# Kernel tuning notes

Measured on AMD Instinct MI355X. Metric: run time of the kernel, lower is better.

The kernel has to match this reference:

```python
import jax, jax.numpy as jnp
import numpy as np

N = 40000      # nodes
E = 640000     # edges
F_IN = 128     # feature_dim
HID = 256      # hidden_dim
OUT = 128      # out_dim
B = 64         # num graphs
HEADS = 4
EPS = 1e-5


def setup_inputs() -> dict:
    key = jax.random.key(0)
    ks = jax.random.split(key, 32)
    s = 0.02
    inp = {
        "x_bb_masked": jax.random.normal(ks[0], (N, F_IN), jnp.float32),
        "x_att_masked": jax.random.normal(ks[1], (N, F_IN), jnp.float32),
        # SAGEConv1: in->hid  (lin_l acts on mean-aggregated neighbors, lin_r on root)
        "W1l": jax.random.normal(ks[2], (HID, F_IN), jnp.float32) * s,
        "b1l": jnp.zeros((HID,), jnp.float32),
        "W1r": jax.random.normal(ks[3], (HID, F_IN), jnp.float32) * s,
        # SAGEConv2: hid->hid
        "W2l": jax.random.normal(ks[4], (HID, HID), jnp.float32) * s,
        "b2l": jnp.zeros((HID,), jnp.float32),
        "W2r": jax.random.normal(ks[5], (HID, HID), jnp.float32) * s,
        # SAGEConv3: hid->out
        "W3l": jax.random.normal(ks[6], (OUT, HID), jnp.float32) * s,
        "b3l": jnp.zeros((OUT,), jnp.float32),
        "W3r": jax.random.normal(ks[7], (OUT, HID), jnp.float32) * s,
        # cross-attention projections
        "Wq": jax.random.normal(ks[8], (HID, F_IN), jnp.float32) * s,
        "bq": jnp.zeros((HID,), jnp.float32),
        "Wk": jax.random.normal(ks[9], (HID, OUT), jnp.float32) * s,
        "bk": jnp.zeros((HID,), jnp.float32),
        "Wv": jax.random.normal(ks[10], (HID, OUT), jnp.float32) * s,
        "bv": jnp.zeros((HID,), jnp.float32),
        # nn.MultiheadAttention packed in-proj and out-proj
        "in_proj_w": jax.random.normal(ks[11], (3 * HID, HID), jnp.float32) * s,
        "in_proj_b": jnp.zeros((3 * HID,), jnp.float32),
        "out_w": jax.random.normal(ks[12], (HID, HID), jnp.float32) * s,
        "out_b": jnp.zeros((HID,), jnp.float32),
        "ln_g": jnp.ones((HID,), jnp.float32),
        "ln_b": jnp.zeros((HID,), jnp.float32),
        "edge_index": jax.random.randint(ks[13], (2, E), 0, N, jnp.int64),
        "batch": jnp.sort(jax.random.randint(ks[14], (N,), 0, B, jnp.int64)),
    }
    return inp


def _sage(x, src, dst, Wl, bl, Wr):
    # mean aggregation of source features at target nodes, then lin_l(agg)+lin_r(x)
    agg = jax.ops.segment_sum(x[src], dst, num_segments=N)          # [N, d]
    cnt = jax.ops.segment_sum(jnp.ones((src.shape[0],), x.dtype), dst, num_segments=N)
    mean = agg / jnp.maximum(cnt, 1.0)[:, None]
    return mean @ Wl.T + bl + x @ Wr.T


def _forward(x_bb_masked, x_att_masked,
             W1l, b1l, W1r, W2l, b2l, W2r, W3l, b3l, W3r,
             Wq, bq, Wk, bk, Wv, bv, in_proj_w, in_proj_b, out_w, out_b,
             ln_g, ln_b, edge_index, batch):
    src, dst = edge_index[0], edge_index[1]
    h = jax.nn.relu(_sage(x_bb_masked, src, dst, W1l, b1l, W1r))
    h = jax.nn.relu(_sage(h, src, dst, W2l, b2l, W2r))
    h = _sage(h, src, dst, W3l, b3l, W3r)                           # [N, OUT]
    # global mean pool per graph
    gsum = jax.ops.segment_sum(h, batch, num_segments=B)            # [B, OUT]
    gcnt = jax.ops.segment_sum(jnp.ones((N,), h.dtype), batch, num_segments=B)
    graph_vec = gsum / jnp.maximum(gcnt, 1.0)[:, None]

    # cross attention: query per node, key/value from its graph vector (seq_len = 1)
    query = x_att_masked @ Wq.T + bq                                # [N, HID]
    gv = graph_vec[batch]                                           # [N, OUT]
    keyt = gv @ Wk.T + bk
    val = gv @ Wv.T + bv
    q = query @ in_proj_w[:HID].T + in_proj_b[:HID]
    k = keyt @ in_proj_w[HID:2 * HID].T + in_proj_b[HID:2 * HID]
    v = val @ in_proj_w[2 * HID:].T + in_proj_b[2 * HID:]
    dh = HID // HEADS
    qh = q.reshape(N, HEADS, dh)
    kh = k.reshape(N, HEADS, dh)
    vh = v.reshape(N, HEADS, dh)
    scores = jnp.sum(qh * kh, axis=-1, keepdims=True) / jnp.sqrt(jnp.asarray(dh, q.dtype))
    w = jax.nn.softmax(scores, axis=-1)                             # length-1 kv -> ones
    attn = (w * vh).reshape(N, HID)
    attn = attn @ out_w.T + out_b
    # LayerNorm
    mu = jnp.mean(attn, axis=-1, keepdims=True)
    var = jnp.mean((attn - mu) ** 2, axis=-1, keepdims=True)
    node_embeddings = (attn - mu) / jnp.sqrt(var + EPS) * ln_g + ln_b
    return graph_vec, node_embeddings


def reference(x_bb_masked, x_att_masked,
              W1l, b1l, W1r, W2l, b2l, W2r, W3l, b3l, W3r,
              Wq, bq, Wk, bk, Wv, bv, in_proj_w, in_proj_b, out_w, out_b,
              ln_g, ln_b, edge_index, batch):
    return _forward(x_bb_masked, x_att_masked,
                    W1l, b1l, W1r, W2l, b2l, W2r, W3l, b3l, W3r,
                    Wq, bq, Wk, bk, Wv, bv, in_proj_w, in_proj_b, out_w, out_b,
                    ln_g, ln_b, edge_index, batch)
```

## Files before the change

kernel.cpp:

```cpp
#include <hip/hip_runtime.h>

#define N_NODES 40000
#define N_EDGES 640000
#define NGRAPH 64

typedef unsigned short u16;
typedef unsigned char u8;
typedef unsigned int u32;
typedef __attribute__((ext_vector_type(2))) float floatx2;
typedef __attribute__((ext_vector_type(4))) float floatx4;
typedef __attribute__((ext_vector_type(8))) short short8;
typedef __attribute__((ext_vector_type(8))) __bf16 bf16x8;

__device__ __forceinline__ float bf2f(u16 u) {
  u32 x = ((u32)u) << 16;
  return __builtin_bit_cast(float, x);
}
__device__ __forceinline__ u16 f2bf(float f) {
  u32 u = __builtin_bit_cast(u32, f);
  u += 0x7fffu + ((u >> 16) & 1u);
  return (u16)(u >> 16);
}
__device__ __forceinline__ uint2 f4tob(float4 v) {
  u32 lo = (u32)f2bf(v.x) | ((u32)f2bf(v.y) << 16);
  u32 hi = (u32)f2bf(v.z) | ((u32)f2bf(v.w) << 16);
  return make_uint2(lo, hi);
}
__device__ __forceinline__ u32 fp8pk_lo(float a, float b, u32 old) {
  return (u32)__builtin_amdgcn_cvt_pk_fp8_f32(a, b, (int)old, false);
}
__device__ __forceinline__ u32 fp8pk_hi(float a, float b, u32 old) {
  return (u32)__builtin_amdgcn_cvt_pk_fp8_f32(a, b, (int)old, true);
}
__device__ __forceinline__ floatx2 fp8up_lo(u32 v) {
  return __builtin_amdgcn_cvt_pk_f32_fp8((int)v, false);
}
__device__ __forceinline__ floatx2 fp8up_hi(u32 v) {
  return __builtin_amdgcn_cvt_pk_f32_fp8((int)v, true);
}
__device__ __forceinline__ void gld16(const void* g, void* l) {
  __builtin_amdgcn_global_load_lds(
      (const __attribute__((address_space(1))) u32*)g,
      (__attribute__((address_space(3))) u32*)l, 16, 0, 0);
}

__global__ __launch_bounds__(256) void k_setup(const float* __restrict__ x_bb, u16* __restrict__ xb,
                                               u8* __restrict__ xq,
                                               const float* __restrict__ W1l, u16* __restrict__ w1l,
                                               const float* __restrict__ W1r, u16* __restrict__ w1r,
                                               const float* __restrict__ W2l, u16* __restrict__ w2l,
                                               const float* __restrict__ W2r, u16* __restrict__ w2r,
                                               const float* __restrict__ W3l, u16* __restrict__ w3s,
                                               const float* __restrict__ W3r, u16* __restrict__ w3r,
                                               int* __restrict__ zbase,
                                               const int* __restrict__ batch, int* __restrict__ gstart) {
  const int tid = blockIdx.x * 256 + threadIdx.x;
  const int nth = gridDim.x * 256;
  for (int i = tid; i < 2 * N_NODES + 8192; i += nth) zbase[i] = 0;
  for (int i = tid; i < N_NODES * 32; i += nth) {
    float4 v = ((const float4*)x_bb)[i];
    ((uint2*)xb)[i] = f4tob(v);
    if (xq) {
      u32 q = fp8pk_lo(v.x, v.y, 0);
      q = fp8pk_hi(v.z, v.w, q);
      ((u32*)xq)[i] = q;
    }
  }
  for (int i = tid; i < 65536; i += nth) {
    const float* s; u16* d; int off;
    if (i < 8192)       { s = W1l; d = w1l; off = i; }
    else if (i < 16384) { s = W1r; d = w1r; off = i - 8192; }
    else if (i < 32768) { s = W2l; d = w2l; off = i - 16384; }
    else if (i < 49152) { s = W2r; d = w2r; off = i - 32768; }
    else if (i < 57344) { s = W3l; d = w3s; off = i - 49152; }
    else                { s = W3r; d = w3r; off = i - 57344; }
    ((uint2*)d)[off] = f4tob(((const float4*)s)[off]);
  }
  if (tid <= NGRAPH) {
    int lo = 0, hi = N_NODES;
    while (lo < hi) { int mid = (lo + hi) >> 1; if (batch[mid] < tid) lo = mid + 1; else hi = mid; }
    gstart[tid] = lo;
  }
}

__global__ void k_hist(const int* __restrict__ ei, int* __restrict__ cnt) {
  int e = blockIdx.x * 256 + threadIdx.x;
  int d = ei[N_EDGES + e];
  atomicAdd(&cnt[d], 1);
}
__global__ void k_blocksum(const int* __restrict__ cnt, int* __restrict__ bsum, int n) {
  __shared__ int s[256];
  int t = threadIdx.x, i = blockIdx.x * 256 + t;
  s[t] = (i < n) ? cnt[i] : 0;
  __syncthreads();
  for (int off = 128; off > 0; off >>= 1) {
    if (t < off) s[t] += s[t + off];
    __syncthreads();
  }
  if (t == 0) bsum[blockIdx.x] = s[0];
}
__global__ void k_scan_small(int* bsum, int n) {
  __shared__ int s[256];
  int t = threadIdx.x;
  int orig = (t < n) ? bsum[t] : 0;
  s[t] = orig;
  __syncthreads();
  for (int off = 1; off < 256; off <<= 1) {
    int v = (t >= off) ? s[t - off] : 0;
    __syncthreads();
    s[t] += v;
    __syncthreads();
  }
  if (t < n) bsum[t] = s[t] - orig;
}
__global__ void k_rowptr(const int* __restrict__ cnt, const int* __restrict__ bsum,
                         int* __restrict__ rowptr, float* __restrict__ invc, int n, int total) {
  __shared__ int s[256];
  int t = threadIdx.x, i = blockIdx.x * 256 + t;
  int c = (i < n) ? cnt[i] : 0;
  s[t] = c;
  __syncthreads();
  for (int off = 1; off < 256; off <<= 1) {
    int v = (t >= off) ? s[t - off] : 0;
    __syncthreads();
    s[t] += v;
    __syncthreads();
  }
  if (i < n) {
    rowptr[i] = bsum[blockIdx.x] + s[t] - c;
    invc[i] = 1.0f / (float)(c > 1 ? c : 1);
  }
  if (i == 0) rowptr[n] = total;
}
__global__ void k_scatter(const int* __restrict__ ei, const int* __restrict__ rowptr,
                          int* __restrict__ cursor, int* __restrict__ perm) {
  int e = blockIdx.x * 256 + threadIdx.x;
  int d = ei[N_EDGES + e];
  int srcn = ei[e];
  int pos = rowptr[d] + atomicAdd(&cursor[d], 1);
  perm[pos] = srcn;
}

template <int D, int MODE, int QT>
__global__ __launch_bounds__(256) void k_agg(const void* __restrict__ xv, u16* __restrict__ outp,
                                             const int* __restrict__ rowptr,
                                             const int* __restrict__ perm,
                                             const float* __restrict__ invc,
                                             const u16* __restrict__ Radd, int nn) {
  int wv = threadIdx.x >> 6, lane = threadIdx.x & 63;
  int node = blockIdx.x * 4 + wv;
  if (node >= nn) return;
  int s = rowptr[node], e = rowptr[node + 1];
  int slot = lane >> 4, lsub = lane & 15;
  constexpr int FR = D / 16;
  float acc[FR];
#pragma unroll
  for (int i = 0; i < FR; ++i) acc[i] = 0.f;

  int p = s + slot;
  if constexpr (QT == 1) {
    const u8* xl = (const u8*)xv + lsub * FR;
    constexpr int NW = FR / 4;
    for (; p + 4 < e; p += 8) {
      int s0 = perm[p], s1 = perm[p + 4];
      const u8* r0 = xl + (size_t)s0 * D;
      const u8* r1 = xl + (size_t)s1 * D;
      u32 wa[NW], wb[NW];
      if constexpr (D == 128) {
        uint2 a = *(const uint2*)r0; wa[0] = a.x; wa[1] = a.y;
        uint2 b = *(const uint2*)r1; wb[0] = b.x; wb[1] = b.y;
      } else {
        uint4 a = *(const uint4*)r0; wa[0] = a.x; wa[1] = a.y; wa[2] = a.z; wa[3] = a.w;
        uint4 b = *(const uint4*)r1; wb[0] = b.x; wb[1] = b.y; wb[2] = b.z; wb[3] = b.w;
      }
#pragma unroll
      for (int j = 0; j < NW; ++j) {
        floatx2 l0 = fp8up_lo(wa[j]), h0 = fp8up_hi(wa[j]);
        floatx2 l1 = fp8up_lo(wb[j]), h1 = fp8up_hi(wb[j]);
        acc[4 * j]     += l0[0] + l1[0];
        acc[4 * j + 1] += l0[1] + l1[1];
        acc[4 * j + 2] += h0[0] + h1[0];
        acc[4 * j + 3] += h0[1] + h1[1];
      }
    }
    if (p < e) {
      int s0 = perm[p];
      const u8* r0 = xl + (size_t)s0 * D;
      u32 wa[NW];
      if constexpr (D == 128) {
        uint2 a = *(const uint2*)r0; wa[0] = a.x; wa[1] = a.y;
      } else {
        uint4 a = *(const uint4*)r0; wa[0] = a.x; wa[1] = a.y; wa[2] = a.z; wa[3] = a.w;
      }
#pragma unroll
      for (int j = 0; j < NW; ++j) {
        floatx2 l0 = fp8up_lo(wa[j]), h0 = fp8up_hi(wa[j]);
        acc[4 * j]     += l0[0];
        acc[4 * j + 1] += l0[1];
        acc[4 * j + 2] += h0[0];
        acc[4 * j + 3] += h0[1];
      }
    }
  } else {
    const u16* xl = (const u16*)xv + lsub * FR;
    for (; p + 4 < e; p += 8) {
      int src0 = perm[p];
      int src1 = perm[p + 4];
      const u16* rp0 = xl + (size_t)src0 * D;
      const u16* rp1 = xl + (size_t)src1 * D;
      if (D == 128) {
        uint4 va = *(const uint4*)rp0;
        uint4 vb = *(const uint4*)rp1;
        u32 wa[4] = {va.x, va.y, va.z, va.w}, wb[4] = {vb.x, vb.y, vb.z, vb.w};
#pragma unroll
        for (int j = 0; j < 4; ++j) {
          acc[2 * j] += __builtin_bit_cast(float, wa[j] << 16) + __builtin_bit_cast(float, wb[j] << 16);
          acc[2 * j + 1] += __builtin_bit_cast(float, wa[j] & 0xffff0000u) + __builtin_bit_cast(float, wb[j] & 0xffff0000u);
        }
      } else {
        uint4 a0 = *(const uint4*)rp0;
        uint4 a1 = *(const uint4*)(rp0 + 8);
        uint4 b0 = *(const uint4*)rp1;
        uint4 b1 = *(const uint4*)(rp1 + 8);
        u32 wa[8] = {a0.x, a0.y, a0.z, a0.w, a1.x, a1.y, a1.z, a1.w};
        u32 wb[8] = {b0.x, b0.y, b0.z, b0.w, b1.x, b1.y, b1.z, b1.w};
#pragma unroll
        for (int j = 0; j < 8; ++j) {
          acc[2 * j] += __builtin_bit_cast(float, wa[j] << 16) + __builtin_bit_cast(float, wb[j] << 16);
          acc[2 * j + 1] += __builtin_bit_cast(float, wa[j] & 0xffff0000u) + __builtin_bit_cast(float, wb[j] & 0xffff0000u);
        }
      }
    }
    if (p < e) {
      int src = perm[p];
      const u16* rp = xl + (size_t)src * D;
      if (D == 128) {
        uint4 va = *(const uint4*)rp;
        u32 wa[4] = {va.x, va.y, va.z, va.w};
#pragma unroll
        for (int j = 0; j < 4; ++j) {
          acc[2 * j] += __builtin_bit_cast(float, wa[j] << 16);
          acc[2 * j + 1] += __builtin_bit_cast(float, wa[j] & 0xffff0000u);
        }
      } else {
        uint4 a0 = *(const uint4*)rp;
        uint4 a1 = *(const uint4*)(rp + 8);
        u32 wa[8] = {a0.x, a0.y, a0.z, a0.w, a1.x, a1.y, a1.z, a1.w};
#pragma unroll
        for (int j = 0; j < 8; ++j) {
          acc[2 * j] += __builtin_bit_cast(float, wa[j] << 16);
          acc[2 * j + 1] += __builtin_bit_cast(float, wa[j] & 0xffff0000u);
        }
      }
    }
  }

#pragma unroll
  for (int i = 0; i < FR; ++i) {
    acc[i] += __shfl_xor(acc[i], 16, 64);
    acc[i] += __shfl_xor(acc[i], 32, 64);
  }

  if (slot == 0) {
    float iv = invc[node];
    float v[FR];
#pragma unroll
    for (int i = 0; i < FR; ++i) v[i] = acc[i] * iv;
    if (MODE == 1) {
      const uint4* rr = (const uint4*)(Radd + (size_t)node * D + lsub * FR);
      uint4 va = rr[0];
      u32 wa[4] = {va.x, va.y, va.z, va.w};
#pragma unroll
      for (int j = 0; j < 4; ++j) {
        v[2 * j] += __builtin_bit_cast(float, wa[j] << 16);
        v[2 * j + 1] += __builtin_bit_cast(float, wa[j] & 0xffff0000u);
      }
    }
    u32 wpk[FR / 2];
#pragma unroll
    for (int i = 0; i < FR / 2; ++i)
      wpk[i] = (u32)f2bf(v[2 * i]) | ((u32)f2bf(v[2 * i + 1]) << 16);
    uint4* o = (uint4*)(outp + (size_t)node * D + lsub * FR);
    o[0] = make_uint4(wpk[0], wpk[1], wpk[2], wpk[3]);
    if (FR == 16) o[1] = make_uint4(wpk[4], wpk[5], wpk[6], wpk[7]);
  }
}

template <int OUTW, int EPI>
__global__ __launch_bounds__(256) void k_gemm(const u16* __restrict__ A1, const u16* __restrict__ W1, int K1,
                                              const u16* __restrict__ A2, const u16* __restrict__ W2, int K2,
                                              const float* __restrict__ bias,
                                              void* __restrict__ out1, void* __restrict__ out2, int M) {
  __shared__ u16 lsA[128 * 64];
  __shared__ u16 lsB[128 * 64];
  const int tid = threadIdx.x, lane = tid & 63, wv = tid >> 6;
  const int wm = wv >> 1, wn = wv & 1;
  const int row0 = blockIdx.x * 128, col0 = blockIdx.y * 128;

  floatx4 acc[4][4];
#pragma unroll
  for (int r = 0; r < 4; ++r)
#pragma unroll
    for (int c = 0; c < 4; ++c) acc[r][c] = 0.f;

  for (int seg = 0; seg < 2; ++seg) {
    const u16* A = seg ? A2 : A1;
    const u16* Wm = seg ? W2 : W1;
    const int K = seg ? K2 : K1;
    if (K == 0) continue;
    for (int k0 = 0; k0 < K; k0 += 64) {
      __syncthreads();
#pragma unroll
      for (int i = 0; i < 4; ++i) {
        int chunk = i * 256 + tid;
        int r = chunk >> 3;
        int kc = chunk & 7;
        int kcs = kc ^ (r & 7);
        int grow = row0 + r;
        grow = grow < M ? grow : M - 1;
        gld16(A + (size_t)grow * K + (k0 + kcs * 8), lsA + (size_t)(i * 256 + wv * 64) * 8);
        int wr = col0 + r;
        gld16(Wm + (size_t)wr * K + (k0 + kcs * 8), lsB + (size_t)(i * 256 + wv * 64) * 8);
      }
      __syncthreads();
#pragma unroll
      for (int kk = 0; kk < 2; ++kk) {
        bf16x8 af[4], bb[4];
        int kc = kk * 4 + (lane >> 4);
#pragma unroll
        for (int r = 0; r < 4; ++r) {
          int row = wm * 64 + r * 16 + (lane & 15);
          af[r] = __builtin_bit_cast(bf16x8, *(const short8*)(lsA + row * 64 + ((kc ^ (row & 7)) << 3)));
        }
#pragma unroll
        for (int c = 0; c < 4; ++c) {
          int row = wn * 64 + c * 16 + (lane & 15);
          bb[c] = __builtin_bit_cast(bf16x8, *(const short8*)(lsB + row * 64 + ((kc ^ (row & 7)) << 3)));
        }
#pragma unroll
        for (int r = 0; r < 4; ++r)
#pragma unroll
          for (int c = 0; c < 4; ++c)
            acc[r][c] = __builtin_amdgcn_mfma_f32_16x16x32_bf16(af[r], bb[c], acc[r][c], 0, 0, 0);
      }
    }
  }

#pragma unroll
  for (int r = 0; r < 4; ++r) {
    int rowb = row0 + wm * 64 + r * 16 + ((lane >> 4) << 2);
#pragma unroll
    for (int c = 0; c < 4; ++c) {
      int col = col0 + wn * 64 + c * 16 + (lane & 15);
#pragma unroll
      for (int j = 0; j < 4; ++j) {
        int gr = rowb + j;
        if (gr < M) {
          float v = acc[r][c][j];
          if constexpr (EPI == 0 || EPI == 1) {
            v += bias[col];
            v = v > 0.f ? v : 0.f;
            ((u16*)out1)[(size_t)gr * OUTW + col] = f2bf(v);
            if constexpr (EPI == 1)
              ((u8*)out2)[(size_t)gr * OUTW + col] = (u8)(fp8pk_lo(v, v, 0) & 0xff);
          } else if constexpr (EPI == 2) {
            if (col < 128) {
              ((u16*)out1)[(size_t)gr * 128 + col] = f2bf(v);
            } else {
              v += bias[col - 128];
              ((u16*)out2)[(size_t)gr * 128 + (col - 128)] = f2bf(v);
            }
          } else {
            if (col < 128) {
              ((u8*)out1)[(size_t)gr * 128 + col] = (u8)(fp8pk_lo(v, v, 0) & 0xff);
            } else {
              v += bias[col - 128];
              ((u16*)out2)[(size_t)gr * 128 + (col - 128)] = f2bf(v);
            }
          }
        }
      }
    }
  }
}

__global__ __launch_bounds__(256) void k_pool_part(const u16* __restrict__ h3,
                                                   const int* __restrict__ batch,
                                                   float* __restrict__ gsum) {
  __shared__ int sb[64];
  int t = threadIdx.x;
  int n0 = blockIdx.x * 64;
  if (t < 64) sb[t] = batch[n0 + t];
  __syncthreads();
  int col = t & 127, sub = t >> 7;
  float acc = 0.f;
  int curg = -1;
  for (int i = sub; i < 64; i += 2) {
    int g = sb[i];
    if (g != curg) {
      if (curg >= 0) atomicAdd(&gsum[curg * 128 + col], acc);
      curg = g;
      acc = 0.f;
    }
    acc += bf2f(h3[(size_t)(n0 + i) * 128 + col]);
  }
  if (curg >= 0) atomicAdd(&gsum[curg * 128 + col], acc);
}

__global__ __launch_bounds__(256) void k_tail(const float* __restrict__ gsum, const int* __restrict__ gstart,
                                              const float* __restrict__ Wv,
                                              const float* __restrict__ bv, const float* __restrict__ ipw,
                                              const float* __restrict__ ipb, const float* __restrict__ outw,
                                              const float* __restrict__ outb, const float* __restrict__ lng,
                                              const float* __restrict__ lnb, float* __restrict__ dout,
                                              float* __restrict__ eout) {
  __shared__ float sa[256], sb[256];
  __shared__ float s_mu, s_var;
  int b = blockIdx.x, t = threadIdx.x;
  if (t < 128) {
    int cg = gstart[b + 1] - gstart[b];
    float mean = gsum[b * 128 + t] / (float)(cg > 1 ? cg : 1);
    sa[t] = mean;
    dout[b * 128 + t] = mean;
  }
  __syncthreads();
  float val = bv[t];
  for (int k = 0; k < 128; ++k) val += sa[k] * Wv[t * 128 + k];
  sb[t] = val;
  __syncthreads();
  float vv = ipb[512 + t];
  for (int k = 0; k < 256; ++k) vv += sb[k] * ipw[(size_t)(512 + t) * 256 + k];
  sa[t] = vv;
  __syncthreads();
  float at = outb[t];
  for (int k = 0; k < 256; ++k) at += sa[k] * outw[t * 256 + k];
  sb[t] = at;
  __syncthreads();
  for (int off = 128; off > 0; off >>= 1) {
    if (t < off) sb[t] += sb[t + off];
    __syncthreads();
  }
  if (t == 0) s_mu = sb[0] * (1.0f / 256.0f);
  __syncthreads();
  float d = at - s_mu;
  sb[t] = d * d;
  __syncthreads();
  for (int off = 128; off > 0; off >>= 1) {
    if (t < off) sb[t] += sb[t + off];
    __syncthreads();
  }
  if (t == 0) s_var = sb[0] * (1.0f / 256.0f);
  __syncthreads();
  float r = 1.0f / sqrtf(s_var + 1e-5f);
  eout[(size_t)b * 256 + t] = d * r * lng[t] + lnb[t];
}

__global__ void k_scat_out(const float* __restrict__ eb, const int* __restrict__ batch,
                           float* __restrict__ dout) {
  int i = blockIdx.x * 256 + threadIdx.x;
  int n = i >> 6, q = i & 63;
  float4 v = ((const float4*)eb)[(size_t)batch[n] * 64 + q];
  ((float4*)(dout + NGRAPH * 128))[i] = v;
}

extern "C" void kernel_launch(void* const* d_in, const int* in_sizes, int n_in,
                              void* d_out, int out_size, void* d_ws, size_t ws_size,
                              hipStream_t stream) {
  (void)in_sizes; (void)n_in; (void)out_size;
  const float* x_bb = (const float*)d_in[0];
  const float* W1l = (const float*)d_in[2];
  const float* b1l = (const float*)d_in[3];
  const float* W1r = (const float*)d_in[4];
  const float* W2l = (const float*)d_in[5];
  const float* b2l = (const float*)d_in[6];
  const float* W2r = (const float*)d_in[7];
  const float* W3l = (const float*)d_in[8];
  const float* b3l = (const float*)d_in[9];
  const float* W3r = (const float*)d_in[10];
  const float* Wv = (const float*)d_in[15];
  const float* bv = (const float*)d_in[16];
  const float* ipw = (const float*)d_in[17];
  const float* ipb = (const float*)d_in[18];
  const float* outw = (const float*)d_in[19];
  const float* outb = (const float*)d_in[20];
  const float* lng = (const float*)d_in[21];
  const float* lnb = (const float*)d_in[22];
  const int* ei = (const int*)d_in[23];
  const int* batch = (const int*)d_in[24];
  float* dout = (float*)d_out;
  char* ws = (char*)d_ws;

  constexpr size_t O_W1L = 0;
  constexpr size_t O_W1R = O_W1L + 256 * 128 * 2;
  constexpr size_t O_W2L = O_W1R + 256 * 128 * 2;
  constexpr size_t O_W2R = O_W2L + 256 * 256 * 2;
  constexpr size_t O_W3L = O_W2R + 256 * 256 * 2;
  constexpr size_t O_W3R = O_W3L + 128 * 256 * 2;
  constexpr size_t O_XB = O_W3R + 128 * 256 * 2;
  constexpr size_t O_MEAN1 = O_XB + (size_t)N_NODES * 128 * 2;
  constexpr size_t O_H1 = O_MEAN1 + (size_t)N_NODES * 128 * 2;
  constexpr size_t O_MEAN2 = O_H1 + (size_t)N_NODES * 256 * 2;
  constexpr size_t O_H2 = O_MEAN2 + (size_t)N_NODES * 256 * 2;
  constexpr size_t O_E = O_H2 + (size_t)N_NODES * 256 * 2;
  constexpr size_t O_CNT = O_E + 64 * 256 * 4;
  constexpr size_t O_CUR = O_CNT + (size_t)N_NODES * 4;
  constexpr size_t O_GSUM = O_CUR + (size_t)N_NODES * 4;
  constexpr size_t O_RP = O_GSUM + 64 * 128 * 4;
  constexpr size_t O_INVC = O_RP + (size_t)(N_NODES + 64) * 4;
  constexpr size_t O_BSUM = O_INVC + (size_t)N_NODES * 4;
  constexpr size_t O_GST = O_BSUM + 1024;
  constexpr size_t O_PERM = O_GST + 512;
  constexpr size_t O_XQ = O_PERM + (size_t)N_EDGES * 4;
  constexpr size_t O_H1Q = O_XQ + (size_t)N_NODES * 128;
  constexpr size_t NEED_FP8 = O_H1Q + (size_t)N_NODES * 256;

  u16* w1l = (u16*)(ws + O_W1L);  u16* w1r = (u16*)(ws + O_W1R);
  u16* w2l = (u16*)(ws + O_W2L);  u16* w2r = (u16*)(ws + O_W2R);
  u16* w3s = (u16*)(ws + O_W3L);  u16* w3r = (u16*)(ws + O_W3R);
  u16* xb = (u16*)(ws + O_XB);
  u16* mean1 = (u16*)(ws + O_MEAN1);
  u16* h1 = (u16*)(ws + O_H1);
  u16* mean2 = (u16*)(ws + O_MEAN2);
  u16* h2 = (u16*)(ws + O_H2);
  u16* Pb = (u16*)(ws + O_XB);
  u16* Rb = (u16*)(ws + O_MEAN1);
  u16* h3b = (u16*)(ws + O_MEAN2);
  float* eb = (float*)(ws + O_E);
  int* cnt = (int*)(ws + O_CNT);
  int* cursor = (int*)(ws + O_CUR);
  float* gsum = (float*)(ws + O_GSUM);
  int* rowptr = (int*)(ws + O_RP);
  float* invc = (float*)(ws + O_INVC);
  int* bsum = (int*)(ws + O_BSUM);
  int* gstart = (int*)(ws + O_GST);
  int* perm = (int*)(ws + O_PERM);
  u8* xq = (u8*)(ws + O_XQ);
  u8* Pq = (u8*)(ws + O_XQ);
  u8* h1q = (u8*)(ws + O_H1Q);

  const bool use_fp8 = (ws_size >= NEED_FP8);
  const int NB = (N_NODES + 255) / 256;
  dim3 blk(256);

  k_setup<<<512, blk, 0, stream>>>(x_bb, xb, use_fp8 ? xq : nullptr,
                                   W1l, w1l, W1r, w1r, W2l, w2l, W2r, w2r,
                                   W3l, w3s, W3r, w3r, cnt, batch, gstart);
  k_hist<<<N_EDGES / 256, blk, 0, stream>>>(ei, cnt);
  k_blocksum<<<NB, blk, 0, stream>>>(cnt, bsum, N_NODES);
  k_scan_small<<<1, blk, 0, stream>>>(bsum, NB);
  k_rowptr<<<NB, blk, 0, stream>>>(cnt, bsum, rowptr, invc, N_NODES, N_EDGES);
  k_scatter<<<N_EDGES / 256, blk, 0, stream>>>(ei, rowptr, cursor, perm);

  if (use_fp8) {
    k_agg<128, 0, 1><<<N_NODES / 4, blk, 0, stream>>>(xq, mean1, rowptr, perm, invc, nullptr, N_NODES);
    k_gemm<256, 1><<<dim3(313, 2), blk, 0, stream>>>(mean1, w1l, 128, xb, w1r, 128, b1l, h1, h1q, N_NODES);
    k_agg<256, 0, 1><<<N_NODES / 4, blk, 0, stream>>>(h1q, mean2, rowptr, perm, invc, nullptr, N_NODES);
    k_gemm<256, 0><<<dim3(313, 2), blk, 0, stream>>>(mean2, w2l, 256, h1, w2r, 256, b2l, h2, nullptr, N_NODES);
    k_gemm<128, 3><<<dim3(313, 2), blk, 0, stream>>>(h2, w3s, 256, nullptr, nullptr, 0, b3l, Pq, Rb, N_NODES);
    k_agg<128, 1, 1><<<N_NODES / 4, blk, 0, stream>>>(Pq, h3b, rowptr, perm, invc, Rb, N_NODES);
  } else {
    k_agg<128, 0, 0><<<N_NODES / 4, blk, 0, stream>>>(xb, mean1, rowptr, perm, invc, nullptr, N_NODES);
    k_gemm<256, 0><<<dim3(313, 2), blk, 0, stream>>>(mean1, w1l, 128, xb, w1r, 128, b1l, h1, nullptr, N_NODES);
    k_agg<256, 0, 0><<<N_NODES / 4, blk, 0, stream>>>(h1, mean2, rowptr, perm, invc, nullptr, N_NODES);
    k_gemm<256, 0><<<dim3(313, 2), blk, 0, stream>>>(mean2, w2l, 256, h1, w2r, 256, b2l, h2, nullptr, N_NODES);
    k_gemm<128, 2><<<dim3(313, 2), blk, 0, stream>>>(h2, w3s, 256, nullptr, nullptr, 0, b3l, Pb, Rb, N_NODES);
    k_agg<128, 1, 0><<<N_NODES / 4, blk, 0, stream>>>(Pb, h3b, rowptr, perm, invc, Rb, N_NODES);
  }

  k_pool_part<<<N_NODES / 64, blk, 0, stream>>>(h3b, batch, gsum);
  k_tail<<<NGRAPH, blk, 0, stream>>>(gsum, gstart, Wv, bv, ipw, ipb, outw, outb, lng, lnb, dout, eb);
  k_scat_out<<<N_NODES * 64 / 256, blk, 0, stream>>>(eb, batch, dout);
}
```

Before: 259.4 us.

## Merge scan kernels, widen GEMM to full 256 columns, fuse pooling into aggregation

Replaces the three-kernel prefix scan with one kernel in which each block recomputes its base by summing all earlier counts. Widens each GEMM block to cover all 256 output columns, so the A tile is loaded once instead of once per column half, at the cost of double the LDS for B and twice the accumulator registers per thread. Fuses the mean-pool into the final aggregation, using LDS atomics when a block's four nodes share one graph and global atomics otherwise. This removes the h3 round trip and the separate pool kernel. The redundant base summation grows with block index, up to about 40K reads for the last block.

```diff
diff --git a/kernel.cpp b/kernel.cpp
--- a/kernel.cpp
+++ b/kernel.cpp
@@ -3,6 +3,7 @@
 #define N_NODES 40000
 #define N_EDGES 640000
 #define NGRAPH 64
+#define NBCH 157
 
 typedef unsigned short u16;
 typedef unsigned char u8;
@@ -88,22 +89,24 @@
   int d = ei[N_EDGES + e];
   atomicAdd(&cnt[d], 1);
 }
-__global__ void k_blocksum(const int* __restrict__ cnt, int* __restrict__ bsum, int n) {
+__global__ __launch_bounds__(256) void k_scanrp(const int* __restrict__ cnt,
+                                                int* __restrict__ rowptr, float* __restrict__ invc) {
   __shared__ int s[256];
-  int t = threadIdx.x, i = blockIdx.x * 256 + t;
-  s[t] = (i < n) ? cnt[i] : 0;
+  __shared__ int s_base;
+  int b = blockIdx.x, t = threadIdx.x;
+  int base = 0;
+  for (int i = t; i < b * 256; i += 256) base += cnt[i];
+  s[t] = base;
   __syncthreads();
   for (int off = 128; off > 0; off >>= 1) {
     if (t < off) s[t] += s[t + off];
     __syncthreads();
   }
-  if (t == 0) bsum[blockIdx.x] = s[0];
-}
-__global__ void k_scan_small(int* bsum, int n) {
-  __shared__ int s[256];
-  int t = threadIdx.x;
-  int orig = (t < n) ? bsum[t] : 0;
-  s[t] = orig;
+  if (t == 0) s_base = s[0];
+  __syncthreads();
+  int i = b * 256 + t;
+  int c = (i < N_NODES) ? cnt[i] : 0;
+  s[t] = c;
   __syncthreads();
   for (int off = 1; off < 256; off <<= 1) {
     int v = (t >= off) ? s[t - off] : 0;
@@ -111,26 +114,11 @@
     s[t] += v;
     __syncthreads();
   }
-  if (t < n) bsum[t] = s[t] - orig;
-}
-__global__ void k_rowptr(const int* __restrict__ cnt, const int* __restrict__ bsum,
-                         int* __restrict__ rowptr, float* __restrict__ invc, int n, int total) {
-  __shared__ int s[256];
-  int t = threadIdx.x, i = blockIdx.x * 256 + t;
-  int c = (i < n) ? cnt[i] : 0;
-  s[t] = c;
-  __syncthreads();
-  for (int off = 1; off < 256; off <<= 1) {
-    int v = (t >= off) ? s[t - off] : 0;
-    __syncthreads();
-    s[t] += v;
-    __syncthreads();
-  }
-  if (i < n) {
-    rowptr[i] = bsum[blockIdx.x] + s[t] - c;
+  if (i < N_NODES) {
+    rowptr[i] = s_base + s[t] - c;
     invc[i] = 1.0f / (float)(c > 1 ? c : 1);
   }
-  if (i == 0) rowptr[n] = total;
+  if (b == 0 && t == 0) rowptr[N_NODES] = N_EDGES;
 }
 __global__ void k_scatter(const int* __restrict__ ei, const int* __restrict__ rowptr,
                           int* __restrict__ cursor, int* __restrict__ perm) {
@@ -146,16 +134,24 @@
                                              const int* __restrict__ rowptr,
                                              const int* __restrict__ perm,
                                              const float* __restrict__ invc,
-                                             const u16* __restrict__ Radd, int nn) {
+                                             const u16* __restrict__ Radd,
+                                             const int* __restrict__ batch,
+                                             float* __restrict__ gsum, int nn) {
+  __shared__ float lacc[128];
+  __shared__ int sgr[2];
   int wv = threadIdx.x >> 6, lane = threadIdx.x & 63;
   int node = blockIdx.x * 4 + wv;
-  if (node >= nn) return;
   int s = rowptr[node], e = rowptr[node + 1];
   int slot = lane >> 4, lsub = lane & 15;
   constexpr int FR = D / 16;
   float acc[FR];
 #pragma unroll
   for (int i = 0; i < FR; ++i) acc[i] = 0.f;
+
+  if constexpr (MODE == 2) {
+    if (threadIdx.x < 128) lacc[threadIdx.x] = 0.f;
+    if (threadIdx.x == 0) { sgr[0] = batch[blockIdx.x * 4]; sgr[1] = batch[blockIdx.x * 4 + 3]; }
+  }
 
   int p = s + slot;
   if constexpr (QT == 1) {
@@ -261,13 +257,29 @@
     acc[i] += __shfl_xor(acc[i], 32, 64);
   }
 
-  if (slot == 0) {
-    float iv = invc[node];
-    float v[FR];
-#pragma unroll
-    for (int i = 0; i < FR; ++i) v[i] = acc[i] * iv;
-    if (MODE == 1) {
-      const uint4* rr = (const uint4*)(Radd + (size_t)node * D + lsub * FR);
+  if constexpr (MODE == 0) {
+    if (slot == 0) {
+      float iv = invc[node];
+      float v[FR];
+#pragma unroll
+      for (int i = 0; i < FR; ++i) v[i] = acc[i] * iv;
+      u32 wpk[FR / 2];
+#pragma unroll
+      for (int i = 0; i < FR / 2; ++i)
+        wpk[i] = (u32)f2bf(v[2 * i]) | ((u32)f2bf(v[2 * i + 1]) << 16);
+      uint4* o = (uint4*)(outp + (size_t)node * D + lsub * FR);
+      o[0] = make_uint4(wpk[0], wpk[1], wpk[2], wpk[3]);
+      if (FR == 16) o[1] = make_uint4(wpk[4], wpk[5], wpk[6], wpk[7]);
+    }
+  } else {
+    __syncthreads();
+    bool uni = (sgr[0] == sgr[1]);
+    if (slot == 0) {
+      float iv = invc[node];
+      float v[8];
+#pragma unroll
+      for (int i = 0; i < 8; ++i) v[i] = acc[i] * iv;
+      const uint4* rr = (const uint4*)(Radd + (size_t)node * 128 + lsub * 8);
       uint4 va = rr[0];
       u32 wa[4] = {va.x, va.y, va.z, va.w};
 #pragma unroll
@@ -275,33 +287,36 @@
         v[2 * j] += __builtin_bit_cast(float, wa[j] << 16);
         v[2 * j + 1] += __builtin_bit_cast(float, wa[j] & 0xffff0000u);
       }
-    }
-    u32 wpk[FR / 2];
-#pragma unroll
-    for (int i = 0; i < FR / 2; ++i)
-      wpk[i] = (u32)f2bf(v[2 * i]) | ((u32)f2bf(v[2 * i + 1]) << 16);
-    uint4* o = (uint4*)(outp + (size_t)node * D + lsub * FR);
-    o[0] = make_uint4(wpk[0], wpk[1], wpk[2], wpk[3]);
-    if (FR == 16) o[1] = make_uint4(wpk[4], wpk[5], wpk[6], wpk[7]);
-  }
-}
-
-template <int OUTW, int EPI>
+      if (uni) {
+#pragma unroll
+        for (int j = 0; j < 8; ++j) atomicAdd(&lacc[lsub * 8 + j], v[j]);
+      } else {
+        int g = batch[node];
+#pragma unroll
+        for (int j = 0; j < 8; ++j) atomicAdd(&gsum[g * 128 + lsub * 8 + j], v[j]);
+      }
+    }
+    __syncthreads();
+    if (uni && threadIdx.x < 128) atomicAdd(&gsum[sgr[0] * 128 + threadIdx.x], lacc[threadIdx.x]);
+  }
+}
+
+template <int EPI>
 __global__ __launch_bounds__(256) void k_gemm(const u16* __restrict__ A1, const u16* __restrict__ W1, int K1,
                                               const u16* __restrict__ A2, const u16* __restrict__ W2, int K2,
                                               const float* __restrict__ bias,
                                               void* __restrict__ out1, void* __restrict__ out2, int M) {
   __shared__ u16 lsA[128 * 64];
-  __shared__ u16 lsB[128 * 64];
+  __shared__ u16 lsB[256 * 64];
   const int tid = threadIdx.x, lane = tid & 63, wv = tid >> 6;
   const int wm = wv >> 1, wn = wv & 1;
-  const int row0 = blockIdx.x * 128, col0 = blockIdx.y * 128;
-
-  floatx4 acc[4][4];
+  const int row0 = blockIdx.x * 128;
+
+  floatx4 acc[4][8];
 #pragma unroll
   for (int r = 0; r < 4; ++r)
 #pragma unroll
-    for (int c = 0; c < 4; ++c) acc[r][c] = 0.f;
+    for (int c = 0; c < 8; ++c) acc[r][c] = 0.f;
 
   for (int seg = 0; seg < 2; ++seg) {
     const u16* A = seg ? A2 : A1;
@@ -319,13 +334,19 @@
         int grow = row0 + r;
         grow = grow < M ? grow : M - 1;
         gld16(A + (size_t)grow * K + (k0 + kcs * 8), lsA + (size_t)(i * 256 + wv * 64) * 8);
-        int wr = col0 + r;
-        gld16(Wm + (size_t)wr * K + (k0 + kcs * 8), lsB + (size_t)(i * 256 + wv * 64) * 8);
+      }
+#pragma unroll
+      for (int i = 0; i < 8; ++i) {
+        int chunk = i * 256 + tid;
+        int r = chunk >> 3;
+        int kc = chunk & 7;
+        int kcs = kc ^ (r & 7);
+        gld16(Wm + (size_t)r * K + (k0 + kcs * 8), lsB + (size_t)(i * 256 + wv * 64) * 8);
       }
       __syncthreads();
 #pragma unroll
       for (int kk = 0; kk < 2; ++kk) {
-        bf16x8 af[4], bb[4];
+        bf16x8 af[4], bb[8];
         int kc = kk * 4 + (lane >> 4);
 #pragma unroll
         for (int r = 0; r < 4; ++r) {
@@ -333,14 +354,14 @@
           af[r] = __builtin_bit_cast(bf16x8, *(const short8*)(lsA + row * 64 + ((kc ^ (row & 7)) << 3)));
         }
 #pragma unroll
-        for (int c = 0; c < 4; ++c) {
-          int row = wn * 64 + c * 16 + (lane & 15);
+        for (int c = 0; c < 8; ++c) {
+          int row = wn * 128 + c * 16 + (lane & 15);
           bb[c] = __builtin_bit_cast(bf16x8, *(const short8*)(lsB + row * 64 + ((kc ^ (row & 7)) << 3)));
         }
 #pragma unroll
         for (int r = 0; r < 4; ++r)
 #pragma unroll
-          for (int c = 0; c < 4; ++c)
+          for (int c = 0; c < 8; ++c)
             acc[r][c] = __builtin_amdgcn_mfma_f32_16x16x32_bf16(af[r], bb[c], acc[r][c], 0, 0, 0);
       }
     }
@@ -350,8 +371,8 @@
   for (int r = 0; r < 4; ++r) {
     int rowb = row0 + wm * 64 + r * 16 + ((lane >> 4) << 2);
 #pragma unroll
-    for (int c = 0; c < 4; ++c) {
-      int col = col0 + wn * 64 + c * 16 + (lane & 15);
+    for (int c = 0; c < 8; ++c) {
+      int col = wn * 128 + c * 16 + (lane & 15);
 #pragma unroll
       for (int j = 0; j < 4; ++j) {
         int gr = rowb + j;
@@ -360,9 +381,9 @@
           if constexpr (EPI == 0 || EPI == 1) {
             v += bias[col];
             v = v > 0.f ? v : 0.f;
-            ((u16*)out1)[(size_t)gr * OUTW + col] = f2bf(v);
+            ((u16*)out1)[(size_t)gr * 256 + col] = f2bf(v);
             if constexpr (EPI == 1)
-              ((u8*)out2)[(size_t)gr * OUTW + col] = (u8)(fp8pk_lo(v, v, 0) & 0xff);
+              ((u8*)out2)[(size_t)gr * 256 + col] = (u8)(fp8pk_lo(v, v, 0) & 0xff);
           } else if constexpr (EPI == 2) {
             if (col < 128) {
               ((u16*)out1)[(size_t)gr * 128 + col] = f2bf(v);
@@ -382,29 +403,6 @@
       }
     }
   }
-}
-
-__global__ __launch_bounds__(256) void k_pool_part(const u16* __restrict__ h3,
-                                                   const int* __restrict__ batch,
-                                                   float* __restrict__ gsum) {
-  __shared__ int sb[64];
-  int t = threadIdx.x;
-  int n0 = blockIdx.x * 64;
-  if (t < 64) sb[t] = batch[n0 + t];
-  __syncthreads();
-  int col = t & 127, sub = t >> 7;
-  float acc = 0.f;
-  int curg = -1;
-  for (int i = sub; i < 64; i += 2) {
-    int g = sb[i];
-    if (g != curg) {
-      if (curg >= 0) atomicAdd(&gsum[curg * 128 + col], acc);
-      curg = g;
-      acc = 0.f;
-    }
-    acc += bf2f(h3[(size_t)(n0 + i) * 128 + col]);
-  }
-  if (curg >= 0) atomicAdd(&gsum[curg * 128 + col], acc);
 }
 
 __global__ __launch_bounds__(256) void k_tail(const float* __restrict__ gsum, const int* __restrict__ gstart,
@@ -507,8 +505,7 @@
   constexpr size_t O_GSUM = O_CUR + (size_t)N_NODES * 4;
   constexpr size_t O_RP = O_GSUM + 64 * 128 * 4;
   constexpr size_t O_INVC = O_RP + (size_t)(N_NODES + 64) * 4;
-  constexpr size_t O_BSUM = O_INVC + (size_t)N_NODES * 4;
-  constexpr size_t O_GST = O_BSUM + 1024;
+  constexpr size_t O_GST = O_INVC + (size_t)N_NODES * 4;
   constexpr size_t O_PERM = O_GST + 512;
   constexpr size_t O_XQ = O_PERM + (size_t)N_EDGES * 4;
   constexpr size_t O_H1Q = O_XQ + (size_t)N_NODES * 128;
@@ -524,14 +521,12 @@
   u16* h2 = (u16*)(ws + O_H2);
   u16* Pb = (u16*)(ws + O_XB);
   u16* Rb = (u16*)(ws + O_MEAN1);
-  u16* h3b = (u16*)(ws + O_MEAN2);
   float* eb = (float*)(ws + O_E);
   int* cnt = (int*)(ws + O_CNT);
   int* cursor = (int*)(ws + O_CUR);
   float* gsum = (float*)(ws + O_GSUM);
   int* rowptr = (int*)(ws + O_RP);
   float* invc = (float*)(ws + O_INVC);
-  int* bsum = (int*)(ws + O_BSUM);
   int* gstart = (int*)(ws + O_GST);
   int* perm = (int*)(ws + O_PERM);
   u8* xq = (u8*)(ws + O_XQ);
@@ -539,35 +534,31 @@
   u8* h1q = (u8*)(ws + O_H1Q);
 
   const bool use_fp8 = (ws_size >= NEED_FP8);
-  const int NB = (N_NODES + 255) / 256;
   dim3 blk(256);
 
   k_setup<<<512, blk, 0, stream>>>(x_bb, xb, use_fp8 ? xq : nullptr,
                                    W1l, w1l, W1r, w1r, W2l, w2l, W2r, w2r,
                                    W3l, w3s, W3r, w3r, cnt, batch, gstart);
   k_hist<<<N_EDGES / 256, blk, 0, stream>>>(ei, cnt);
-  k_blocksum<<<NB, blk, 0, stream>>>(cnt, bsum, N_NODES);
-  k_scan_small<<<1, blk, 0, stream>>>(bsum, NB);
-  k_rowptr<<<NB, blk, 0, stream>>>(cnt, bsum, rowptr, invc, N_NODES, N_EDGES);
+  k_scanrp<<<NBCH, blk, 0, stream>>>(cnt, rowptr, invc);
   k_scatter<<<N_EDGES / 256, blk, 0, stream>>>(ei, rowptr, cursor, perm);
 
   if (use_fp8) {
-    k_agg<128, 0, 1><<<N_NODES / 4, blk, 0, stream>>>(xq, mean1, rowptr, perm, invc, nullptr, N_NODES);
-    k_gemm<256, 1><<<dim3(313, 2), blk, 0, stream>>>(mean1, w1l, 128, xb, w1r, 128, b1l, h1, h1q, N_NODES);
-    k_agg<256, 0, 1><<<N_NODES / 4, blk, 0, stream>>>(h1q, mean2, rowptr, perm, invc, nullptr, N_NODES);
-    k_gemm<256, 0><<<dim3(313, 2), blk, 0, stream>>>(mean2, w2l, 256, h1, w2r, 256, b2l, h2, nullptr, N_NODES);
-    k_gemm<128, 3><<<dim3(313, 2), blk, 0, stream>>>(h2, w3s, 256, nullptr, nullptr, 0, b3l, Pq, Rb, N_NODES);
-    k_agg<128, 1, 1><<<N_NODES / 4, blk, 0, stream>>>(Pq, h3b, rowptr, perm, invc, Rb, N_NODES);
+    k_agg<128, 0, 1><<<N_NODES / 4, blk, 0, stream>>>(xq, mean1, rowptr, perm, invc, nullptr, batch, nullptr, N_NODES);
+    k_gemm<1><<<313, blk, 0, stream>>>(mean1, w1l, 128, xb, w1r, 128, b1l, h1, h1q, N_NODES);
+    k_agg<256, 0, 1><<<N_NODES / 4, blk, 0, stream>>>(h1q, mean2, rowptr, perm, invc, nullptr, batch, nullptr, N_NODES);
+    k_gemm<0><<<313, blk, 0, stream>>>(mean2, w2l, 256, h1, w2r, 256, b2l, h2, nullptr, N_NODES);
+    k_gemm<3><<<313, blk, 0, stream>>>(h2, w3s, 256, nullptr, nullptr, 0, b3l, Pq, Rb, N_NODES);
+    k_agg<128, 2, 1><<<N_NODES / 4, blk, 0, stream>>>(Pq, nullptr, rowptr, perm, invc, Rb, batch, gsum, N_NODES);
   } else {
-    k_agg<128, 0, 0><<<N_NODES / 4, blk, 0, stream>>>(xb, mean1, rowptr, perm, invc, nullptr, N_NODES);
-    k_gemm<256, 0><<<dim3(313, 2), blk, 0, stream>>>(mean1, w1l, 128, xb, w1r, 128, b1l, h1, nullptr, N_NODES);
-    k_agg<256, 0, 0><<<N_NODES / 4, blk, 0, stream>>>(h1, mean2, rowptr, perm, invc, nullptr, N_NODES);
-    k_gemm<256, 0><<<dim3(313, 2), blk, 0, stream>>>(mean2, w2l, 256, h1, w2r, 256, b2l, h2, nullptr, N_NODES);
-    k_gemm<128, 2><<<dim3(313, 2), blk, 0, stream>>>(h2, w3s, 256, nullptr, nullptr, 0, b3l, Pb, Rb, N_NODES);
-    k_agg<128, 1, 0><<<N_NODES / 4, blk, 0, stream>>>(Pb, h3b, rowptr, perm, invc, Rb, N_NODES);
-  }
-
-  k_pool_part<<<N_NODES / 64, blk, 0, stream>>>(h3b, batch, gsum);
+    k_agg<128, 0, 0><<<N_NODES / 4, blk, 0, stream>>>(xb, mean1, rowptr, perm, invc, nullptr, batch, nullptr, N_NODES);
+    k_gemm<0><<<313, blk, 0, stream>>>(mean1, w1l, 128, xb, w1r, 128, b1l, h1, nullptr, N_NODES);
+    k_agg<256, 0, 0><<<N_NODES / 4, blk, 0, stream>>>(h1, mean2, rowptr, perm, invc, nullptr, batch, nullptr, N_NODES);
+    k_gemm<0><<<313, blk, 0, stream>>>(mean2, w2l, 256, h1, w2r, 256, b2l, h2, nullptr, N_NODES);
+    k_gemm<2><<<313, blk, 0, stream>>>(h2, w3s, 256, nullptr, nullptr, 0, b3l, Pb, Rb, N_NODES);
+    k_agg<128, 2, 0><<<N_NODES / 4, blk, 0, stream>>>(Pb, nullptr, rowptr, perm, invc, Rb, batch, gsum, N_NODES);
+  }
+
   k_tail<<<NGRAPH, blk, 0, stream>>>(gsum, gstart, Wv, bv, ipw, ipb, outw, outb, lng, lnb, dout, eb);
   k_scat_out<<<N_NODES * 64 / 256, blk, 0, stream>>>(eb, batch, dout);
 }
```

Measured after the change: 385.3 us. +48.5%, slower.
